# Optimization experiments

Measured on AMD Instinct MI355X. Metric: run time of the kernel, lower is better.

The kernel has to match this reference:

```python
import jax, jax.numpy as jnp
import numpy as np

TOPK = 2

def setup_inputs() -> dict:
    key = jax.random.key(0)
    k1, k2, k3, k4 = jax.random.split(key, 4)
    T, H, F, E = 2048, 1024, 4096, 8
    x = jax.random.normal(k1, (T, H), dtype=jnp.float32)
    router_weight = jax.random.normal(k2, (H, E), dtype=jnp.float32) * (1.0 / np.sqrt(H))
    w1 = jax.random.normal(k3, (E, H, F), dtype=jnp.float32) * (1.0 / np.sqrt(H))
    w2 = jax.random.normal(k4, (E, F, H), dtype=jnp.float32) * (1.0 / np.sqrt(F))
    return {"x": x, "router_weight": router_weight, "w1": w1, "w2": w2}


def reference(x, router_weight, w1, w2):
    # x: [T, H] tokens; w1: [E, H, F]; w2: [E, F, H]
    T, H = x.shape
    E = w1.shape[0]
    K = TOPK
    M = T * K  # total dispatched token copies

    # --- TopKRouter (Megatron default: top-k over logits, softmax over selected) ---
    logits = x @ router_weight                      # [T, E]
    top_logits, top_idx = jax.lax.top_k(logits, K)  # [T, K]
    probs = jax.nn.softmax(top_logits, axis=-1)     # [T, K]

    # --- AG-scatter: group token copies by expert (flux grouped-GEMM layout) ---
    flat_expert = top_idx.reshape(-1)               # [M], token-major
    token_id = jnp.repeat(jnp.arange(T), K)         # [M]
    order = jnp.argsort(flat_expert)                # stable sort by expert id
    xg = x[token_id[order]]                         # [M, H] grouped inputs
    eg = flat_expert[order]                         # [M] expert of each slot

    # --- grouped GEMM1 + fused GELU, grouped GEMM2 (exact, via expert masking) ---
    # Rows not belonging to expert e are zeroed; gelu(0)=0 and 0@w2=0, so the
    # accumulated buffers are exactly the grouped-GEMM results.
    gelu_buf = jnp.zeros((M, w1.shape[2]), dtype=x.dtype)
    y = jnp.zeros((M, H), dtype=x.dtype)
    for e in range(E):
        mask = (eg == e)[:, None].astype(x.dtype)
        ge = jax.nn.gelu((xg * mask) @ w1[e], approximate=False)  # [M, F]
        gelu_buf = gelu_buf + ge
        y = y + ge @ w2[e]

    # --- gather + reduce: weighted combine of the K expert outputs per token ---
    pg = probs.reshape(-1)[order]                   # [M]
    mlp_output = jax.ops.segment_sum(y * pg[:, None], token_id[order], num_segments=T)
    return (mlp_output, gelu_buf)
```

## Files before the change

kernel.cpp:

```cpp
#include <hip/hip_runtime.h>
#include <hip/hip_bf16.h>
#include <stdint.h>

typedef unsigned short u16;
typedef unsigned int u32;
typedef __attribute__((ext_vector_type(8))) short short8;
typedef __attribute__((ext_vector_type(4))) float f32x4;

#define T_TOK 2048
#define H_DIM 1024
#define F_DIM 4096
#define E_NUM 8
#define M_SLOT 4096
#define MAXTILES 40
#define KSPLIT 4

__device__ __forceinline__ u16 f2bf(float f){
  union { float f; u32 u; } v; v.f = f;
  return (u16)((v.u + 0x7FFFu + ((v.u >> 16) & 1u)) >> 16);
}

__device__ __forceinline__ void gload_lds16(const void* g, void* l){
  __builtin_amdgcn_global_load_lds(
      (const __attribute__((address_space(1))) u32*)g,
      (__attribute__((address_space(3))) u32*)l, 16, 0, 0);
}

__global__ __launch_bounds__(256) void router_kernel(
    const float* __restrict__ x, const float* __restrict__ rw,
    int* __restrict__ tok_e, float* __restrict__ tok_p){
  __shared__ float wlds[E_NUM * H_DIM];
  int tid = threadIdx.x;
  for (int i = tid; i < H_DIM * E_NUM; i += 256){
    int h = i >> 3, e = i & 7;
    wlds[e * H_DIM + h] = rw[i];
  }
  __syncthreads();
  int wave = tid >> 6, lane = tid & 63;
  int t = blockIdx.x * 4 + wave;
  const float* xr = x + (size_t)t * H_DIM;
  float acc[E_NUM];
  #pragma unroll
  for (int e = 0; e < E_NUM; e++) acc[e] = 0.f;
  for (int i = 0; i < H_DIM / 64; i++){
    float xv = xr[lane + 64 * i];
    #pragma unroll
    for (int e = 0; e < E_NUM; e++) acc[e] += xv * wlds[e * H_DIM + lane + 64 * i];
  }
  #pragma unroll
  for (int e = 0; e < E_NUM; e++){
    float r = acc[e];
    #pragma unroll
    for (int off = 32; off; off >>= 1) r += __shfl_xor(r, off, 64);
    acc[e] = r;
  }
  if (lane == 0){
    float l0 = acc[0]; int e0 = 0;
    #pragma unroll
    for (int e = 1; e < E_NUM; e++) if (acc[e] > l0){ l0 = acc[e]; e0 = e; }
    float l1 = -INFINITY; int e1 = 0;
    #pragma unroll
    for (int e = 0; e < E_NUM; e++) if (e != e0 && acc[e] > l1){ l1 = acc[e]; e1 = e; }
    float ex = expf(l1 - l0);
    float inv = 1.f / (1.f + ex);
    tok_e[2*t] = e0; tok_e[2*t+1] = e1;
    tok_p[2*t] = inv; tok_p[2*t+1] = ex * inv;
  }
}

__global__ void hist_kernel(const int* __restrict__ tok_e, u32* __restrict__ partial){
  int lane = threadIdx.x & 63;
  int m = blockIdx.x * 64 + lane;
  int e = tok_e[m];
  #pragma unroll
  for (int ee = 0; ee < E_NUM; ee++){
    unsigned long long mk = __ballot(e == ee);
    if (lane == ee) partial[blockIdx.x * E_NUM + ee] = (u32)__popcll(mk);
  }
}

__global__ void scan_kernel(const u32* __restrict__ partial, u32* __restrict__ baseb,
                            int4* __restrict__ tiles, int* __restrict__ ntiles){
  int lane = threadIdx.x;
  u32 exc[E_NUM], tot[E_NUM];
  #pragma unroll
  for (int e = 0; e < E_NUM; e++){
    u32 v = partial[lane * E_NUM + e];
    u32 own = v;
    #pragma unroll
    for (int off = 1; off < 64; off <<= 1){
      u32 tu = __shfl_up(v, off, 64);
      if (lane >= off) v += tu;
    }
    exc[e] = v - own;
    tot[e] = __shfl(v, 63, 64);
  }
  u32 offs[E_NUM + 1]; offs[0] = 0;
  #pragma unroll
  for (int e = 0; e < E_NUM; e++) offs[e+1] = offs[e] + tot[e];
  #pragma unroll
  for (int e = 0; e < E_NUM; e++) baseb[lane * E_NUM + e] = offs[e] + exc[e];
  if (lane == 0){
    int nt = 0;
    for (int e = 0; e < E_NUM; e++){
      int cnt = (int)tot[e];
      for (int r0 = 0; r0 < cnt; r0 += 128){
        tiles[nt] = make_int4((int)offs[e] + r0, min(128, cnt - r0), e, 0);
        nt++;
      }
    }
    *ntiles = nt;
  }
}

__global__ void scatter_kernel(const int* __restrict__ tok_e, const u32* __restrict__ baseb,
                               int* __restrict__ dest){
  int lane = threadIdx.x & 63;
  int m = blockIdx.x * 64 + lane;
  int e = tok_e[m];
  unsigned long long eq = 0;
  #pragma unroll
  for (int ee = 0; ee < E_NUM; ee++){
    unsigned long long mk = __ballot(e == ee);
    if (e == ee) eq = mk;
  }
  u32 rank = (u32)__popcll(eq & ((1ull << lane) - 1ull));
  dest[m] = (int)(baseb[blockIdx.x * E_NUM + e] + rank);
}

template<int R, int C>
__device__ __forceinline__ void transpose_body(const float* __restrict__ in,
                                               u16* __restrict__ out,
                                               int cx, int ry, int e,
                                               u16 (*tile)[66]){
  const float* ip = in + (size_t)e * R * C;
  u16* op = out + (size_t)e * R * C;
  int c0 = cx * 64, r0 = ry * 64;
  int tr = threadIdx.x >> 4, tc = threadIdx.x & 15;
  #pragma unroll
  for (int i = 0; i < 4; i++){
    int r = tr + i * 16;
    float4 v = *(const float4*)(ip + (size_t)(r0 + r) * C + c0 + tc * 4);
    tile[r][tc*4+0] = f2bf(v.x); tile[r][tc*4+1] = f2bf(v.y);
    tile[r][tc*4+2] = f2bf(v.z); tile[r][tc*4+3] = f2bf(v.w);
  }
  __syncthreads();
  #pragma unroll
  for (int i = 0; i < 4; i++){
    int c = tr + i * 16;
    ushort4 o;
    o.x = tile[tc*4+0][c]; o.y = tile[tc*4+1][c];
    o.z = tile[tc*4+2][c]; o.w = tile[tc*4+3][c];
    *(ushort4*)(op + (size_t)(c0 + c) * R + r0 + tc * 4) = o;
  }
}

template<int N, int KSTRIDE, int NT, bool GELU_EP>
__device__ __forceinline__ void gemm_body(
    u16* As, u16* Bs,
    const u16* __restrict__ A, const u16* __restrict__ Bt,
    const int4* __restrict__ tiles, const int* __restrict__ ntiles_p,
    float* __restrict__ outF, u16* __restrict__ outB, size_t zstride,
    int colBlk, int tileBlk, int z){
  if (tileBlk >= *ntiles_p) return;
  int4 ti = tiles[tileBlk];
  int row0 = ti.x, nrows = ti.y, e = ti.z;
  int col0 = colBlk * 128;
  size_t kofs = (size_t)z * ((size_t)NT * 64);
  const u16* Be = Bt + (size_t)e * N * KSTRIDE;
  float* outFz = outF + (size_t)z * zstride;

  int lane = threadIdx.x & 63, wid = threadIdx.x >> 6;
  int wr = wid >> 1, wc = wid & 1;

  f32x4 acc[4][4];
  #pragma unroll
  for (int m = 0; m < 4; m++)
    #pragma unroll
    for (int n = 0; n < 4; n++) acc[m][n] = (f32x4)0.f;

  int srow = (wid << 3) + (lane >> 3);
  int skx  = ((lane & 7) * 16) ^ ((lane >> 3) << 4);

  for (int kt = 0; kt < NT; kt++){
    size_t kb = kofs + (size_t)kt * 64;
    #pragma unroll
    for (int i = 0; i < 4; i++){
      int row = i * 32 + srow;
      gload_lds16((const char*)(A  + (size_t)(row0 + row) * KSTRIDE + kb) + skx,
                  As + i * 2048 + wid * 512);
      gload_lds16((const char*)(Be + (size_t)(col0 + row) * KSTRIDE + kb) + skx,
                  Bs + i * 2048 + wid * 512);
    }
    __syncthreads();
    short8 a[4][2], b[4][2];
    #pragma unroll
    for (int m = 0; m < 4; m++){
      int row = wr * 64 + m * 16 + (lane & 15);
      #pragma unroll
      for (int kk = 0; kk < 2; kk++){
        int byte_ = row * 128 + ((kk * 64 + (lane >> 4) * 16) ^ ((row & 7) << 4));
        a[m][kk] = *(const short8*)((const char*)As + byte_);
      }
    }
    #pragma unroll
    for (int n = 0; n < 4; n++){
      int row = wc * 64 + n * 16 + (lane & 15);
      #pragma unroll
      for (int kk = 0; kk < 2; kk++){
        int byte_ = row * 128 + ((kk * 64 + (lane >> 4) * 16) ^ ((row & 7) << 4));
        b[n][kk] = *(const short8*)((const char*)Bs + byte_);
      }
    }
    #pragma unroll
    for (int m = 0; m < 4; m++)
      #pragma unroll
      for (int n = 0; n < 4; n++)
        #pragma unroll
        for (int kk = 0; kk < 2; kk++)
          acc[m][n] = __builtin_amdgcn_mfma_f32_16x16x32_bf16(a[m][kk], b[n][kk], acc[m][n], 0, 0, 0);
    __syncthreads();
  }

  #pragma unroll
  for (int m = 0; m < 4; m++){
    int rloc = wr * 64 + m * 16 + (lane >> 4) * 4;
    #pragma unroll
    for (int j = 0; j < 4; j++){
      int rr = rloc + j;
      if (rr < nrows){
        size_t rowg = (size_t)(row0 + rr);
        #pragma unroll
        for (int n = 0; n < 4; n++){
          int cc = col0 + wc * 64 + n * 16 + (lane & 15);
          float v = acc[m][n][j];
          if (GELU_EP){
            float g = v * 0.5f * (1.f + erff(v * 0.70710678118f));
            outFz[rowg * N + cc] = g;
            outB[rowg * N + cc] = f2bf(g);
          } else {
            outFz[rowg * N + cc] = v;
          }
        }
      }
    }
  }
}

__global__ __launch_bounds__(256) void gather_tw1_kernel(
    const float* __restrict__ x, const int* __restrict__ dest,
    u16* __restrict__ xg, const float* __restrict__ w1, u16* __restrict__ w1t){
  __shared__ __align__(16) u16 tile[64][66];
  int bid = blockIdx.x;
  if (bid < M_SLOT){
    int d = dest[bid];
    const float4* xr = (const float4*)(x + (size_t)(bid >> 1) * H_DIM);
    float4 v = xr[threadIdx.x];
    ushort4 o;
    o.x = f2bf(v.x); o.y = f2bf(v.y); o.z = f2bf(v.z); o.w = f2bf(v.w);
    ((ushort4*)(xg + (size_t)d * H_DIM))[threadIdx.x] = o;
  } else {
    int tb = bid - M_SLOT;
    transpose_body<H_DIM, F_DIM>(w1, w1t, tb & 63, (tb >> 6) & 15, tb >> 10, tile);
  }
}

__global__ __launch_bounds__(256, 4) void gemm1_tw2_kernel(
    const u16* __restrict__ xg, const u16* __restrict__ w1t,
    const int4* __restrict__ tiles, const int* __restrict__ ntiles,
    float* __restrict__ out_gelu, u16* __restrict__ gb,
    const float* __restrict__ w2, u16* __restrict__ w2t){
  __shared__ __align__(16) u16 sh[2 * 128 * 64];
  int bid = blockIdx.x;
  if (bid < 32 * MAXTILES){
    gemm_body<F_DIM, H_DIM, 16, true>(sh, sh + 8192, xg, w1t, tiles, ntiles,
                                      out_gelu, gb, 0, bid & 31, bid >> 5, 0);
  } else {
    int tb = bid - 32 * MAXTILES;
    transpose_body<F_DIM, H_DIM>(w2, w2t, tb & 15, (tb >> 4) & 63, tb >> 10,
                                 (u16(*)[66])sh);
  }
}

__global__ __launch_bounds__(256, 4) void gemm2_kernel(
    const u16* __restrict__ gb, const u16* __restrict__ w2t,
    const int4* __restrict__ tiles, const int* __restrict__ ntiles,
    float* __restrict__ ypart){
  __shared__ __align__(16) u16 sh[2 * 128 * 64];
  gemm_body<H_DIM, F_DIM, 16, false>(sh, sh + 8192, gb, w2t, tiles, ntiles,
                                     ypart, nullptr, (size_t)M_SLOT * H_DIM,
                                     blockIdx.x, blockIdx.y, blockIdx.z);
}

__global__ __launch_bounds__(256) void combine_kernel(const float* __restrict__ yp,
                                                      const int* __restrict__ dest,
                                                      const float* __restrict__ tok_p,
                                                      float* __restrict__ out){
  int t = blockIdx.x;
  int d0 = dest[2*t], d1 = dest[2*t+1];
  float p0 = tok_p[2*t], p1 = tok_p[2*t+1];
  float4 r; r.x = 0.f; r.y = 0.f; r.z = 0.f; r.w = 0.f;
  #pragma unroll
  for (int s = 0; s < KSPLIT; s++){
    float4 a = ((const float4*)(yp + ((size_t)s * M_SLOT + d0) * H_DIM))[threadIdx.x];
    float4 b = ((const float4*)(yp + ((size_t)s * M_SLOT + d1) * H_DIM))[threadIdx.x];
    r.x += p0*a.x + p1*b.x; r.y += p0*a.y + p1*b.y;
    r.z += p0*a.z + p1*b.z; r.w += p0*a.w + p1*b.w;
  }
  ((float4*)(out + (size_t)t * H_DIM))[threadIdx.x] = r;
}

extern "C" void kernel_launch(void* const* d_in, const int* in_sizes, int n_in,
                              void* d_out, int out_size, void* d_ws, size_t ws_size,
                              hipStream_t stream) {
  const float* x  = (const float*)d_in[0];
  const float* rw = (const float*)d_in[1];
  const float* w1 = (const float*)d_in[2];
  const float* w2 = (const float*)d_in[3];
  float* out_mlp  = (float*)d_out;
  float* out_gelu = (float*)d_out + (size_t)T_TOK * H_DIM;

  char* ws = (char*)d_ws;
  u16*   w1t   = (u16*)(ws + 0);
  float* ypart = (float*)(ws + 0);
  u16*   w2t   = (u16*)(ws + 67108864);
  u16*   xg    = (u16*)(ws + 134217728);
  u16*   gb    = (u16*)(ws + 143130624);
  char*  small = ws + 178782208;
  int*   tok_e = (int*)(small);
  float* tok_p = (float*)(small + 16384);
  int*   dest  = (int*)(small + 32768);
  u32*   partial = (u32*)(small + 49152);
  u32*   baseb   = (u32*)(small + 51200);
  int4*  tiles   = (int4*)(small + 53248);
  int*   ntiles  = (int*)(small + 54272);

  router_kernel<<<T_TOK/4, 256, 0, stream>>>(x, rw, tok_e, tok_p);
  hist_kernel<<<M_SLOT/64, 64, 0, stream>>>(tok_e, partial);
  scan_kernel<<<1, 64, 0, stream>>>(partial, baseb, tiles, ntiles);
  scatter_kernel<<<M_SLOT/64, 64, 0, stream>>>(tok_e, baseb, dest);
  gather_tw1_kernel<<<M_SLOT + 8192, 256, 0, stream>>>(x, dest, xg, w1, w1t);
  gemm1_tw2_kernel<<<32 * MAXTILES + 8192, 256, 0, stream>>>(
      xg, w1t, tiles, ntiles, out_gelu, gb, w2, w2t);
  gemm2_kernel<<<dim3(H_DIM/128, MAXTILES, KSPLIT), 256, 0, stream>>>(
      gb, w2t, tiles, ntiles, ypart);
  combine_kernel<<<T_TOK, 256, 0, stream>>>(ypart, dest, tok_p, out_mlp);
}
```

Before: 236.0 us.

## Co-schedule w1 transpose with router and merge hist/scan/scatter into one kernel

Moves the w1 fp32-to-bf16 transpose blocks from the gather kernel into the router launch, so the transpose runs alongside routing instead of waiting behind the dispatch chain. The histogram, scan and scatter steps are merged into a single one-block kernel that keeps partial counts in LDS, cutting two launches and their global round trips. The gather then runs as its own small kernel. The trade-off is that the router blocks now reserve 32KB of LDS in the combined launch, which may limit occupancy for the transpose blocks, and the merged pack step runs serially on one block.

```diff
diff --git a/kernel.cpp b/kernel.cpp
--- a/kernel.cpp
+++ b/kernel.cpp
@@ -24,108 +24,6 @@
   __builtin_amdgcn_global_load_lds(
       (const __attribute__((address_space(1))) u32*)g,
       (__attribute__((address_space(3))) u32*)l, 16, 0, 0);
-}
-
-__global__ __launch_bounds__(256) void router_kernel(
-    const float* __restrict__ x, const float* __restrict__ rw,
-    int* __restrict__ tok_e, float* __restrict__ tok_p){
-  __shared__ float wlds[E_NUM * H_DIM];
-  int tid = threadIdx.x;
-  for (int i = tid; i < H_DIM * E_NUM; i += 256){
-    int h = i >> 3, e = i & 7;
-    wlds[e * H_DIM + h] = rw[i];
-  }
-  __syncthreads();
-  int wave = tid >> 6, lane = tid & 63;
-  int t = blockIdx.x * 4 + wave;
-  const float* xr = x + (size_t)t * H_DIM;
-  float acc[E_NUM];
-  #pragma unroll
-  for (int e = 0; e < E_NUM; e++) acc[e] = 0.f;
-  for (int i = 0; i < H_DIM / 64; i++){
-    float xv = xr[lane + 64 * i];
-    #pragma unroll
-    for (int e = 0; e < E_NUM; e++) acc[e] += xv * wlds[e * H_DIM + lane + 64 * i];
-  }
-  #pragma unroll
-  for (int e = 0; e < E_NUM; e++){
-    float r = acc[e];
-    #pragma unroll
-    for (int off = 32; off; off >>= 1) r += __shfl_xor(r, off, 64);
-    acc[e] = r;
-  }
-  if (lane == 0){
-    float l0 = acc[0]; int e0 = 0;
-    #pragma unroll
-    for (int e = 1; e < E_NUM; e++) if (acc[e] > l0){ l0 = acc[e]; e0 = e; }
-    float l1 = -INFINITY; int e1 = 0;
-    #pragma unroll
-    for (int e = 0; e < E_NUM; e++) if (e != e0 && acc[e] > l1){ l1 = acc[e]; e1 = e; }
-    float ex = expf(l1 - l0);
-    float inv = 1.f / (1.f + ex);
-    tok_e[2*t] = e0; tok_e[2*t+1] = e1;
-    tok_p[2*t] = inv; tok_p[2*t+1] = ex * inv;
-  }
-}
-
-__global__ void hist_kernel(const int* __restrict__ tok_e, u32* __restrict__ partial){
-  int lane = threadIdx.x & 63;
-  int m = blockIdx.x * 64 + lane;
-  int e = tok_e[m];
-  #pragma unroll
-  for (int ee = 0; ee < E_NUM; ee++){
-    unsigned long long mk = __ballot(e == ee);
-    if (lane == ee) partial[blockIdx.x * E_NUM + ee] = (u32)__popcll(mk);
-  }
-}
-
-__global__ void scan_kernel(const u32* __restrict__ partial, u32* __restrict__ baseb,
-                            int4* __restrict__ tiles, int* __restrict__ ntiles){
-  int lane = threadIdx.x;
-  u32 exc[E_NUM], tot[E_NUM];
-  #pragma unroll
-  for (int e = 0; e < E_NUM; e++){
-    u32 v = partial[lane * E_NUM + e];
-    u32 own = v;
-    #pragma unroll
-    for (int off = 1; off < 64; off <<= 1){
-      u32 tu = __shfl_up(v, off, 64);
-      if (lane >= off) v += tu;
-    }
-    exc[e] = v - own;
-    tot[e] = __shfl(v, 63, 64);
-  }
-  u32 offs[E_NUM + 1]; offs[0] = 0;
-  #pragma unroll
-  for (int e = 0; e < E_NUM; e++) offs[e+1] = offs[e] + tot[e];
-  #pragma unroll
-  for (int e = 0; e < E_NUM; e++) baseb[lane * E_NUM + e] = offs[e] + exc[e];
-  if (lane == 0){
-    int nt = 0;
-    for (int e = 0; e < E_NUM; e++){
-      int cnt = (int)tot[e];
-      for (int r0 = 0; r0 < cnt; r0 += 128){
-        tiles[nt] = make_int4((int)offs[e] + r0, min(128, cnt - r0), e, 0);
-        nt++;
-      }
-    }
-    *ntiles = nt;
-  }
-}
-
-__global__ void scatter_kernel(const int* __restrict__ tok_e, const u32* __restrict__ baseb,
-                               int* __restrict__ dest){
-  int lane = threadIdx.x & 63;
-  int m = blockIdx.x * 64 + lane;
-  int e = tok_e[m];
-  unsigned long long eq = 0;
-  #pragma unroll
-  for (int ee = 0; ee < E_NUM; ee++){
-    unsigned long long mk = __ballot(e == ee);
-    if (e == ee) eq = mk;
-  }
-  u32 rank = (u32)__popcll(eq & ((1ull << lane) - 1ull));
-  dest[m] = (int)(baseb[blockIdx.x * E_NUM + e] + rank);
 }
 
 template<int R, int C>
@@ -153,6 +51,129 @@
     o.z = tile[tc*4+2][c]; o.w = tile[tc*4+3][c];
     *(ushort4*)(op + (size_t)(c0 + c) * R + r0 + tc * 4) = o;
   }
+}
+
+__global__ __launch_bounds__(256) void router_tw1_kernel(
+    const float* __restrict__ x, const float* __restrict__ rw,
+    int* __restrict__ tok_e, float* __restrict__ tok_p,
+    const float* __restrict__ w1, u16* __restrict__ w1t){
+  __shared__ __align__(16) char shbuf[E_NUM * H_DIM * 4];
+  int bid = blockIdx.x;
+  if (bid >= T_TOK / 4){
+    int tb = bid - T_TOK / 4;
+    transpose_body<H_DIM, F_DIM>(w1, w1t, tb & 63, (tb >> 6) & 15, tb >> 10,
+                                 (u16(*)[66])shbuf);
+    return;
+  }
+  float* wlds = (float*)shbuf;
+  int tid = threadIdx.x;
+  for (int i = tid; i < H_DIM * E_NUM; i += 256){
+    int h = i >> 3, e = i & 7;
+    wlds[e * H_DIM + h] = rw[i];
+  }
+  __syncthreads();
+  int wave = tid >> 6, lane = tid & 63;
+  int t = bid * 4 + wave;
+  const float* xr = x + (size_t)t * H_DIM;
+  float acc[E_NUM];
+  #pragma unroll
+  for (int e = 0; e < E_NUM; e++) acc[e] = 0.f;
+  for (int i = 0; i < H_DIM / 64; i++){
+    float xv = xr[lane + 64 * i];
+    #pragma unroll
+    for (int e = 0; e < E_NUM; e++) acc[e] += xv * wlds[e * H_DIM + lane + 64 * i];
+  }
+  #pragma unroll
+  for (int e = 0; e < E_NUM; e++){
+    float r = acc[e];
+    #pragma unroll
+    for (int off = 32; off; off >>= 1) r += __shfl_xor(r, off, 64);
+    acc[e] = r;
+  }
+  if (lane == 0){
+    float l0 = acc[0]; int e0 = 0;
+    #pragma unroll
+    for (int e = 1; e < E_NUM; e++) if (acc[e] > l0){ l0 = acc[e]; e0 = e; }
+    float l1 = -INFINITY; int e1 = 0;
+    #pragma unroll
+    for (int e = 0; e < E_NUM; e++) if (e != e0 && acc[e] > l1){ l1 = acc[e]; e1 = e; }
+    float ex = expf(l1 - l0);
+    float inv = 1.f / (1.f + ex);
+    tok_e[2*t] = e0; tok_e[2*t+1] = e1;
+    tok_p[2*t] = inv; tok_p[2*t+1] = ex * inv;
+  }
+}
+
+__global__ __launch_bounds__(256) void route_pack_kernel(
+    const int* __restrict__ tok_e, int* __restrict__ dest,
+    int4* __restrict__ tiles, int* __restrict__ ntiles){
+  __shared__ u32 part[64][E_NUM];
+  __shared__ u32 base[64][E_NUM];
+  int tid = threadIdx.x, lane = tid & 63, wv = tid >> 6;
+  for (int c = wv; c < 64; c += 4){
+    int e = tok_e[c * 64 + lane];
+    #pragma unroll
+    for (int ee = 0; ee < E_NUM; ee++){
+      unsigned long long mk = __ballot(e == ee);
+      if (lane == ee) part[c][ee] = (u32)__popcll(mk);
+    }
+  }
+  __syncthreads();
+  if (wv == 0){
+    u32 exc[E_NUM], tot[E_NUM];
+    #pragma unroll
+    for (int e = 0; e < E_NUM; e++){
+      u32 v = part[lane][e];
+      u32 own = v;
+      #pragma unroll
+      for (int off = 1; off < 64; off <<= 1){
+        u32 tu = __shfl_up(v, off, 64);
+        if (lane >= off) v += tu;
+      }
+      exc[e] = v - own;
+      tot[e] = __shfl(v, 63, 64);
+    }
+    u32 offs[E_NUM + 1]; offs[0] = 0;
+    #pragma unroll
+    for (int e = 0; e < E_NUM; e++) offs[e+1] = offs[e] + tot[e];
+    #pragma unroll
+    for (int e = 0; e < E_NUM; e++) base[lane][e] = offs[e] + exc[e];
+    if (lane == 0){
+      int nt = 0;
+      for (int e = 0; e < E_NUM; e++){
+        int cnt = (int)tot[e];
+        for (int r0 = 0; r0 < cnt; r0 += 128){
+          tiles[nt] = make_int4((int)offs[e] + r0, min(128, cnt - r0), e, 0);
+          nt++;
+        }
+      }
+      *ntiles = nt;
+    }
+  }
+  __syncthreads();
+  for (int c = wv; c < 64; c += 4){
+    int e = tok_e[c * 64 + lane];
+    unsigned long long eq = 0;
+    #pragma unroll
+    for (int ee = 0; ee < E_NUM; ee++){
+      unsigned long long mk = __ballot(e == ee);
+      if (e == ee) eq = mk;
+    }
+    u32 rank = (u32)__popcll(eq & ((1ull << lane) - 1ull));
+    dest[c * 64 + lane] = (int)(base[c][e] + rank);
+  }
+}
+
+__global__ __launch_bounds__(256) void gather_kernel(const float* __restrict__ x,
+                                                     const int* __restrict__ dest,
+                                                     u16* __restrict__ xg){
+  int m = blockIdx.x;
+  int d = dest[m];
+  const float4* xr = (const float4*)(x + (size_t)(m >> 1) * H_DIM);
+  float4 v = xr[threadIdx.x];
+  ushort4 o;
+  o.x = f2bf(v.x); o.y = f2bf(v.y); o.z = f2bf(v.z); o.w = f2bf(v.w);
+  ((ushort4*)(xg + (size_t)d * H_DIM))[threadIdx.x] = o;
 }
 
 template<int N, int KSTRIDE, int NT, bool GELU_EP>
@@ -247,24 +268,6 @@
   }
 }
 
-__global__ __launch_bounds__(256) void gather_tw1_kernel(
-    const float* __restrict__ x, const int* __restrict__ dest,
-    u16* __restrict__ xg, const float* __restrict__ w1, u16* __restrict__ w1t){
-  __shared__ __align__(16) u16 tile[64][66];
-  int bid = blockIdx.x;
-  if (bid < M_SLOT){
-    int d = dest[bid];
-    const float4* xr = (const float4*)(x + (size_t)(bid >> 1) * H_DIM);
-    float4 v = xr[threadIdx.x];
-    ushort4 o;
-    o.x = f2bf(v.x); o.y = f2bf(v.y); o.z = f2bf(v.z); o.w = f2bf(v.w);
-    ((ushort4*)(xg + (size_t)d * H_DIM))[threadIdx.x] = o;
-  } else {
-    int tb = bid - M_SLOT;
-    transpose_body<H_DIM, F_DIM>(w1, w1t, tb & 63, (tb >> 6) & 15, tb >> 10, tile);
-  }
-}
-
 __global__ __launch_bounds__(256, 4) void gemm1_tw2_kernel(
     const u16* __restrict__ xg, const u16* __restrict__ w1t,
     const int4* __restrict__ tiles, const int* __restrict__ ntiles,
@@ -330,16 +333,12 @@
   int*   tok_e = (int*)(small);
   float* tok_p = (float*)(small + 16384);
   int*   dest  = (int*)(small + 32768);
-  u32*   partial = (u32*)(small + 49152);
-  u32*   baseb   = (u32*)(small + 51200);
-  int4*  tiles   = (int4*)(small + 53248);
-  int*   ntiles  = (int*)(small + 54272);
-
-  router_kernel<<<T_TOK/4, 256, 0, stream>>>(x, rw, tok_e, tok_p);
-  hist_kernel<<<M_SLOT/64, 64, 0, stream>>>(tok_e, partial);
-  scan_kernel<<<1, 64, 0, stream>>>(partial, baseb, tiles, ntiles);
-  scatter_kernel<<<M_SLOT/64, 64, 0, stream>>>(tok_e, baseb, dest);
-  gather_tw1_kernel<<<M_SLOT + 8192, 256, 0, stream>>>(x, dest, xg, w1, w1t);
+  int4*  tiles = (int4*)(small + 53248);
+  int*   ntiles = (int*)(small + 54272);
+
+  router_tw1_kernel<<<T_TOK/4 + 8192, 256, 0, stream>>>(x, rw, tok_e, tok_p, w1, w1t);
+  route_pack_kernel<<<1, 256, 0, stream>>>(tok_e, dest, tiles, ntiles);
+  gather_kernel<<<M_SLOT, 256, 0, stream>>>(x, dest, xg);
   gemm1_tw2_kernel<<<32 * MAXTILES + 8192, 256, 0, stream>>>(
       xg, w1t, tiles, ntiles, out_gelu, gb, w2, w2t);
   gemm2_kernel<<<dim3(H_DIM/128, MAXTILES, KSPLIT), 256, 0, stream>>>(
```

Measured after the change: 236.0 us. About the same (+0.0%).
